# Performance work log

Measured on AMD Instinct MI355X. Metric: run time of the kernel, lower is better.

The kernel has to match this reference:

```python
import jax, jax.numpy as jnp
import numpy as np

B, N, K = 8, 4096, 64          # graphs, nodes per graph, clusters
E_PER = 65536                   # edges per graph (avg degree 16)
EPS = 1e-15


def gcn_conv(x, W, b, src, dst, num_nodes):
    """PyG GCNConv: add self-loops, symmetric deg^-1/2 normalization, sum-aggregate at dst."""
    h = x @ W
    loop = jnp.arange(num_nodes, dtype=src.dtype)
    s_all = jnp.concatenate([src, loop])
    d_all = jnp.concatenate([dst, loop])
    deg = jax.ops.segment_sum(jnp.ones(d_all.shape[0], dtype=h.dtype), d_all, num_segments=num_nodes)
    dis = jnp.where(deg > 0, jax.lax.rsqrt(deg), 0.0)
    msg = h[s_all] * (dis[s_all] * dis[d_all])[:, None]
    return jax.ops.segment_sum(msg, d_all, num_segments=num_nodes) + b


def setup_inputs() -> dict:
    key = jax.random.key(0)
    ks = jax.random.split(key, 12)
    F_in, H, F_out = 128, 128, 128
    x = jax.random.normal(ks[0], (B * N, F_in), dtype=jnp.float32)
    # within-graph random edges, then offset to global node ids
    local = jax.random.randint(ks[1], (2, B * E_PER), 0, N, dtype=jnp.int32)
    offs = jnp.repeat(jnp.arange(B, dtype=jnp.int32) * N, E_PER)
    edge_index = local + offs[None, :]
    batch = jnp.repeat(jnp.arange(B, dtype=jnp.int32), N)

    def lin(k, i, o):
        return (jax.random.normal(k, (i, o), dtype=jnp.float32) / np.float32(np.sqrt(i)))

    return {
        "x": x, "edge_index": edge_index, "batch": batch,
        "W1": lin(ks[2], F_in, H), "b1": jnp.zeros((H,), jnp.float32),
        "W2": lin(ks[3], H, H),    "b2": jnp.zeros((H,), jnp.float32),
        "Wa1": lin(ks[4], H, H),   "ba1": jnp.zeros((H,), jnp.float32),
        "Wa2": lin(ks[5], H, K),   "ba2": jnp.zeros((K,), jnp.float32),
        "Wo": lin(ks[6], H, F_out), "bo": jnp.zeros((F_out,), jnp.float32),
    }


def reference(x, edge_index, batch, W1, b1, W2, b2, Wa1, ba1, Wa2, ba2, Wo, bo):
    num_nodes = B * N
    src, dst = edge_index[0], edge_index[1]
    # two GCN layers (dropout inactive in eval mode)
    h = jax.nn.relu(gcn_conv(x, W1, b1, src, dst, num_nodes))
    h = gcn_conv(h, W2, b2, src, dst, num_nodes)
    # assignment MLP + softmax (module applies softmax; dense_mincut_pool re-applies it)
    s = jax.nn.softmax(jnp.tanh(h @ Wa1 + ba1) @ Wa2 + ba2, axis=-1)
    # to_dense_adj: scatter edges into [B, N, N]
    g = src // N
    adj = jnp.zeros((B, N, N), h.dtype).at[g, src % N, dst % N].add(1.0)
    # to_dense_batch: equal-size graphs -> reshape (mask all True)
    x_d = h.reshape(B, N, -1)
    s_d = jax.nn.softmax(s.reshape(B, N, K), axis=-1)  # PyG internal softmax (double softmax, faithful)
    # dense_mincut_pool
    out = jnp.einsum('bnk,bnf->bkf', s_d, x_d)              # s^T x : [B,K,F]
    As = jnp.einsum('bnm,bmk->bnk', adj, s_d)
    out_adj = jnp.einsum('bnk,bnj->bkj', s_d, As)           # s^T A s : [B,K,K]
    mincut_num = jnp.trace(out_adj, axis1=-2, axis2=-1)
    d_flat = adj.sum(-1)                                    # node degrees
    mincut_den = jnp.einsum('bnk,bn,bnk->b', s_d, d_flat, s_d)  # trace(s^T D s)
    mincut_loss = jnp.mean(-(mincut_num / mincut_den))
    ss = jnp.einsum('bnk,bnj->bkj', s_d, s_d)
    ss_n = jnp.linalg.norm(ss, axis=(-1, -2), keepdims=True)
    i_s = jnp.eye(K, dtype=ss.dtype)
    ortho_loss = jnp.mean(jnp.linalg.norm(ss / ss_n - i_s / jnp.sqrt(jnp.float32(K)), axis=(-1, -2)))
    # zero diagonal + symmetric degree normalization of pooled adj
    out_adj = out_adj * (1.0 - i_s)
    d = jnp.sqrt(out_adj.sum(-1))[:, None, :] + EPS         # [B,1,K]
    out_adj = out_adj / d / jnp.swapaxes(d, 1, 2)
    # output projection
    pooled_x = jax.nn.relu(out.reshape(-1, out.shape[-1]) @ Wo + bo)  # [B*K, F_out]
    pooled_batch = jnp.repeat(jnp.arange(B), K)
    # pooled_adj returned densely: pooled_edge_index == nonzero(pooled_adj > 0) (dynamic shape)
    return pooled_x, out_adj, pooled_batch, mincut_loss, ortho_loss
```

## Files before the change

kernel.cpp:

```cpp
#include <hip/hip_runtime.h>

#define NNODES 32768
#define NEDGES 524288
#define KCL 64
#define CPG 16

typedef _Float16 half8v __attribute__((ext_vector_type(8)));
typedef _Float16 half4v __attribute__((ext_vector_type(4)));
typedef float floatx4 __attribute__((ext_vector_type(4)));

#define WT1_OFF   0
#define WT2_OFF   16384
#define WTA1_OFF  32768
#define WTA2_OFF  49152
#define WTO_OFF   57344
#define WT_TOTAL  73728

__device__ __forceinline__ float wave_sum(float v) {
#pragma unroll
  for (int off = 32; off > 0; off >>= 1) v += __shfl_xor(v, off, 64);
  return v;
}

__global__ __launch_bounds__(256) void hist2_kernel(const int* __restrict__ src, const int* __restrict__ dst,
                                                    int* __restrict__ pIn,
                                                    const float* __restrict__ W1, const float* __restrict__ W2,
                                                    const float* __restrict__ Wa1, const float* __restrict__ Wa2,
                                                    const float* __restrict__ Wo, _Float16* __restrict__ wt16) {
  __shared__ int hIn[4096];
  const int t = threadIdx.x;
  const int g = blockIdx.x & 7;
  const int chunk = blockIdx.x >> 3;
  const int ebase = (g << 16) + (chunk << 12);
  const int nbase = g << 12;
  for (int i = t; i < 4096; i += 256) hIn[i] = 0;
  __syncthreads();
  {
    int tg = blockIdx.x * 256 + t;
#pragma unroll
    for (int i = 0; i < 3; i++) {
      int id = tg + i * 32768;
      if (id < WT_TOTAL) {
        const float* W; int base, BN;
        if (id < 16384)      { W = W1;  base = WT1_OFF;  BN = 128; }
        else if (id < 32768) { W = W2;  base = WT2_OFF;  BN = 128; }
        else if (id < 49152) { W = Wa1; base = WTA1_OFF; BN = 128; }
        else if (id < 57344) { W = Wa2; base = WTA2_OFF; BN = 64; }
        else                 { W = Wo;  base = WTO_OFF;  BN = 128; }
        int m = id - base;
        int k = m / BN, n = m % BN;
        wt16[base + n * 128 + k] = (_Float16)W[m];
      }
    }
  }
  const int4* dst4 = reinterpret_cast<const int4*>(dst + ebase);
#pragma unroll
  for (int i = 0; i < 4; ++i) {
    int4 d = dst4[i * 256 + t];
    atomicAdd(&hIn[d.x - nbase], 1);
    atomicAdd(&hIn[d.y - nbase], 1);
    atomicAdd(&hIn[d.z - nbase], 1);
    atomicAdd(&hIn[d.w - nbase], 1);
  }
  __syncthreads();
  int* dIn = pIn + ((size_t)(g * CPG + chunk) << 12);
  for (int i = t; i < 4096; i += 256) dIn[i] = hIn[i];
}

__global__ __launch_bounds__(1024) void scan2_kernel(const int* __restrict__ pIn, int* __restrict__ offs,
                                                     int* __restrict__ cbase, float* __restrict__ dis) {
  __shared__ int part[1024];
  const int t = threadIdx.x;
  const int g = blockIdx.x;
  int tot[4];
  int s = 0;
#pragma unroll
  for (int j = 0; j < 4; ++j) {
    int l = t * 4 + j;
    int cnt = 0;
#pragma unroll
    for (int c = 0; c < CPG; ++c) cnt += pIn[(((size_t)(g * CPG + c)) << 12) + l];
    tot[j] = cnt;
    s += cnt;
  }
  part[t] = s;
  __syncthreads();
  for (int off = 1; off < 1024; off <<= 1) {
    int add = (t >= off) ? part[t - off] : 0;
    __syncthreads();
    part[t] += add;
    __syncthreads();
  }
  int run = (g << 16) + ((t == 0) ? 0 : part[t - 1]);
#pragma unroll
  for (int j = 0; j < 4; ++j) {
    int l = t * 4 + j;
    int n = (g << 12) + l;
    offs[n] = run;
    dis[n] = rsqrtf((float)tot[j] + 1.0f);
    int running = run;
#pragma unroll
    for (int c = 0; c < CPG; ++c) {
      size_t idx = (((size_t)(g * CPG + c)) << 12) + l;
      cbase[idx] = running;
      running += pIn[idx];
    }
    run += tot[j];
  }
  if (g == 0 && t == 0) offs[NNODES] = NEDGES;
}

__global__ __launch_bounds__(256) void scatter2_kernel(const int* __restrict__ src, const int* __restrict__ dst,
                                                       const int* __restrict__ cbase, int* __restrict__ ssrc) {
  __shared__ int cur[4096];
  const int t = threadIdx.x;
  const int g = blockIdx.x & 7;
  const int chunk = blockIdx.x >> 3;
  const int ebase = (g << 16) + (chunk << 12);
  const int nbase = g << 12;
  const int* cb = cbase + ((size_t)(g * CPG + chunk) << 12);
  for (int i = t; i < 4096; i += 256) cur[i] = cb[i];
  __syncthreads();
  const int4* dst4 = reinterpret_cast<const int4*>(dst + ebase);
  const int4* src4 = reinterpret_cast<const int4*>(src + ebase);
#pragma unroll
  for (int i = 0; i < 4; ++i) {
    int4 d = dst4[i * 256 + t];
    int4 s = src4[i * 256 + t];
    int p0 = atomicAdd(&cur[d.x - nbase], 1); ssrc[p0] = s.x;
    int p1 = atomicAdd(&cur[d.y - nbase], 1); ssrc[p1] = s.y;
    int p2 = atomicAdd(&cur[d.z - nbase], 1); ssrc[p2] = s.z;
    int p3 = atomicAdd(&cur[d.w - nbase], 1); ssrc[p3] = s.w;
  }
}

template <int ACT, int BIAS, int SCALE, int AFP32>
__global__ __launch_bounds__(256) void mgemm_kernel(const void* __restrict__ Ain, const _Float16* __restrict__ WT16,
                                                    const float* __restrict__ bias, const float* __restrict__ rowscale,
                                                    _Float16* __restrict__ Cout) {
  __shared__ _Float16 WT[128][136];
  const int t = threadIdx.x;
  const int lane = t & 63;
  const int quad = lane >> 4, l16 = lane & 15;
  const long rowbase = (long)(blockIdx.x & 7) * 4096 + (long)(blockIdx.x >> 3) * 128 + (t >> 6) * 32;
  half8v af[2][4];
#pragma unroll
  for (int rt = 0; rt < 2; rt++)
#pragma unroll
    for (int kt = 0; kt < 4; kt++) {
      if (AFP32) {
        const float* A32 = (const float*)Ain;
        const float* p = A32 + (rowbase + rt * 16 + l16) * 128 + kt * 32 + quad * 8;
        float4 p0 = *reinterpret_cast<const float4*>(p);
        float4 p1 = *reinterpret_cast<const float4*>(p + 4);
        half8v h = {(_Float16)p0.x, (_Float16)p0.y, (_Float16)p0.z, (_Float16)p0.w,
                    (_Float16)p1.x, (_Float16)p1.y, (_Float16)p1.z, (_Float16)p1.w};
        af[rt][kt] = h;
      } else {
        const _Float16* A16 = (const _Float16*)Ain;
        af[rt][kt] = *reinterpret_cast<const half8v*>(A16 + (rowbase + rt * 16 + l16) * 128 + kt * 32 + quad * 8);
      }
    }
#pragma unroll
  for (int i = 0; i < 8; i++) {
    int idx = i * 256 + t;
    int n = idx >> 4, k8 = (idx & 15) << 3;
    *reinterpret_cast<half8v*>(&WT[n][k8]) = *reinterpret_cast<const half8v*>(&WT16[n * 128 + k8]);
  }
  __syncthreads();
  floatx4 acc[2][8];
#pragma unroll
  for (int rt = 0; rt < 2; rt++)
#pragma unroll
    for (int ct = 0; ct < 8; ct++) acc[rt][ct] = {0.f, 0.f, 0.f, 0.f};
#pragma unroll
  for (int kt = 0; kt < 4; kt++) {
    half8v bf[8];
#pragma unroll
    for (int ct = 0; ct < 8; ct++)
      bf[ct] = *reinterpret_cast<const half8v*>(&WT[ct * 16 + l16][kt * 32 + quad * 8]);
#pragma unroll
    for (int rt = 0; rt < 2; rt++)
#pragma unroll
      for (int ct = 0; ct < 8; ct++)
        acc[rt][ct] = __builtin_amdgcn_mfma_f32_16x16x32_f16(af[rt][kt], bf[ct], acc[rt][ct], 0, 0, 0);
  }
#pragma unroll
  for (int rt = 0; rt < 2; rt++) {
#pragma unroll
    for (int r = 0; r < 4; r++) {
      long row = rowbase + rt * 16 + quad * 4 + r;
      float sc = SCALE ? rowscale[row] : 1.f;
#pragma unroll
      for (int ct = 0; ct < 8; ct++) {
        float v = acc[rt][ct][r];
        if (SCALE) v *= sc;
        if (BIAS) v += bias[ct * 16 + l16];
        if (ACT == 1) v = fmaxf(v, 0.f);
        Cout[row * 128 + ct * 16 + l16] = (_Float16)v;
      }
    }
  }
}

__global__ __launch_bounds__(256) void mlp_kernel(const _Float16* __restrict__ h2, const _Float16* __restrict__ wta1,
                                                  const _Float16* __restrict__ wta2, const float* __restrict__ ba1,
                                                  const float* __restrict__ ba2, _Float16* __restrict__ sh) {
  __shared__ _Float16 WT1[128][136];
  __shared__ _Float16 Z[128][136];
  const int t = threadIdx.x;
  const int lane = t & 63;
  const int quad = lane >> 4, l16 = lane & 15;
  const int w = t >> 6;
  const long rowbase = (long)(blockIdx.x & 7) * 4096 + (long)(blockIdx.x >> 3) * 128 + w * 32;
  half8v af[2][4];
#pragma unroll
  for (int rt = 0; rt < 2; rt++)
#pragma unroll
    for (int kt = 0; kt < 4; kt++)
      af[rt][kt] = *reinterpret_cast<const half8v*>(h2 + (rowbase + rt * 16 + l16) * 128 + kt * 32 + quad * 8);
#pragma unroll
  for (int i = 0; i < 8; i++) {
    int idx = i * 256 + t;
    int n = idx >> 4, k8 = (idx & 15) << 3;
    *reinterpret_cast<half8v*>(&WT1[n][k8]) = *reinterpret_cast<const half8v*>(&wta1[n * 128 + k8]);
  }
  __syncthreads();
  {
    floatx4 acc[2][8];
#pragma unroll
    for (int rt = 0; rt < 2; rt++)
#pragma unroll
      for (int ct = 0; ct < 8; ct++) acc[rt][ct] = {0.f, 0.f, 0.f, 0.f};
#pragma unroll
    for (int kt = 0; kt < 4; kt++) {
      half8v bf[8];
#pragma unroll
      for (int ct = 0; ct < 8; ct++)
        bf[ct] = *reinterpret_cast<const half8v*>(&WT1[ct * 16 + l16][kt * 32 + quad * 8]);
#pragma unroll
      for (int rt = 0; rt < 2; rt++)
#pragma unroll
        for (int ct = 0; ct < 8; ct++)
          acc[rt][ct] = __builtin_amdgcn_mfma_f32_16x16x32_f16(af[rt][kt], bf[ct], acc[rt][ct], 0, 0, 0);
    }
#pragma unroll
    for (int rt = 0; rt < 2; rt++)
#pragma unroll
      for (int r = 0; r < 4; r++) {
        int lrow = w * 32 + rt * 16 + quad * 4 + r;
#pragma unroll
        for (int ct = 0; ct < 8; ct++) {
          float v = tanhf(acc[rt][ct][r] + ba1[ct * 16 + l16]);
          Z[lrow][ct * 16 + l16] = (_Float16)v;
        }
      }
  }
  __syncthreads();
#pragma unroll
  for (int i = 0; i < 4; i++) {
    int idx = i * 256 + t;
    int n = idx >> 4, k8 = (idx & 15) << 3;
    *reinterpret_cast<half8v*>(&WT1[n][k8]) = *reinterpret_cast<const half8v*>(&wta2[n * 128 + k8]);
  }
  half8v af2[2][4];
#pragma unroll
  for (int rt = 0; rt < 2; rt++)
#pragma unroll
    for (int kt = 0; kt < 4; kt++)
      af2[rt][kt] = *reinterpret_cast<const half8v*>(&Z[w * 32 + rt * 16 + l16][kt * 32 + quad * 8]);
  __syncthreads();
  floatx4 acc2[2][4];
#pragma unroll
  for (int rt = 0; rt < 2; rt++)
#pragma unroll
    for (int ct = 0; ct < 4; ct++) acc2[rt][ct] = {0.f, 0.f, 0.f, 0.f};
#pragma unroll
  for (int kt = 0; kt < 4; kt++) {
    half8v bf[4];
#pragma unroll
    for (int ct = 0; ct < 4; ct++)
      bf[ct] = *reinterpret_cast<const half8v*>(&WT1[ct * 16 + l16][kt * 32 + quad * 8]);
#pragma unroll
    for (int rt = 0; rt < 2; rt++)
#pragma unroll
      for (int ct = 0; ct < 4; ct++)
        acc2[rt][ct] = __builtin_amdgcn_mfma_f32_16x16x32_f16(af2[rt][kt], bf[ct], acc2[rt][ct], 0, 0, 0);
  }
#pragma unroll
  for (int rt = 0; rt < 2; rt++) {
#pragma unroll
    for (int r = 0; r < 4; r++) {
      long row = rowbase + rt * 16 + quad * 4 + r;
      float v[4];
#pragma unroll
      for (int ct = 0; ct < 4; ct++) v[ct] = acc2[rt][ct][r] + ba2[ct * 16 + l16];
      float m = fmaxf(fmaxf(v[0], v[1]), fmaxf(v[2], v[3]));
#pragma unroll
      for (int off = 1; off <= 8; off <<= 1) m = fmaxf(m, __shfl_xor(m, off, 64));
      float se = 0.f;
#pragma unroll
      for (int ct = 0; ct < 4; ct++) { v[ct] = __expf(v[ct] - m); se += v[ct]; }
#pragma unroll
      for (int off = 1; off <= 8; off <<= 1) se += __shfl_xor(se, off, 64);
      float inv = 1.0f / se;
#pragma unroll
      for (int ct = 0; ct < 4; ct++) v[ct] *= inv;
      float m2 = fmaxf(fmaxf(v[0], v[1]), fmaxf(v[2], v[3]));
#pragma unroll
      for (int off = 1; off <= 8; off <<= 1) m2 = fmaxf(m2, __shfl_xor(m2, off, 64));
      float se2 = 0.f;
#pragma unroll
      for (int ct = 0; ct < 4; ct++) { v[ct] = __expf(v[ct] - m2); se2 += v[ct]; }
#pragma unroll
      for (int off = 1; off <= 8; off <<= 1) se2 += __shfl_xor(se2, off, 64);
      float inv2 = 1.0f / se2;
#pragma unroll
      for (int ct = 0; ct < 4; ct++) sh[row * 64 + ct * 16 + l16] = (_Float16)(v[ct] * inv2);
    }
  }
}

__global__ __launch_bounds__(256) void aggregate_kernel(const _Float16* __restrict__ hs, const float* __restrict__ dis,
                                                        const int* __restrict__ offs, const int* __restrict__ ssrc,
                                                        const float* __restrict__ bias, _Float16* __restrict__ outh,
                                                        int relu) {
  const int lane = threadIdx.x & 63;
  const int b = blockIdx.x;
  const int node = ((b & 7) << 12) + ((b >> 3) << 2) + (threadIdx.x >> 6);
  const int q = lane >> 4;
  const int fl = (lane & 15) * 8;
  const int e0 = offs[node], e1 = offs[node + 1];
  float fa[8];
#pragma unroll
  for (int j = 0; j < 8; j++) fa[j] = 0.f;
  int e = e0;
  for (; e + 16 <= e1; e += 16) {
    int s0 = ssrc[e + q];
    int s1 = ssrc[e + 4 + q];
    int s2 = ssrc[e + 8 + q];
    int s3 = ssrc[e + 12 + q];
    half8v v0 = *reinterpret_cast<const half8v*>(hs + (size_t)s0 * 128 + fl);
    half8v v1 = *reinterpret_cast<const half8v*>(hs + (size_t)s1 * 128 + fl);
    half8v v2 = *reinterpret_cast<const half8v*>(hs + (size_t)s2 * 128 + fl);
    half8v v3 = *reinterpret_cast<const half8v*>(hs + (size_t)s3 * 128 + fl);
#pragma unroll
    for (int j = 0; j < 8; j++) fa[j] += (float)v0[j] + (float)v1[j] + (float)v2[j] + (float)v3[j];
  }
  if (e < e1) {
    int last = e1 - 1;
    int s[4]; bool m[4];
#pragma unroll
    for (int jj = 0; jj < 4; jj++) {
      int idx = e + jj * 4 + q;
      m[jj] = idx < e1;
      int sv = ssrc[idx < last ? idx : last];
      s[jj] = m[jj] ? sv : node;
    }
#pragma unroll
    for (int jj = 0; jj < 4; jj++) {
      half8v v = *reinterpret_cast<const half8v*>(hs + (size_t)s[jj] * 128 + fl);
      if (m[jj]) {
#pragma unroll
        for (int j = 0; j < 8; j++) fa[j] += (float)v[j];
      }
    }
  }
#pragma unroll
  for (int j = 0; j < 8; j++) {
    fa[j] += __shfl_xor(fa[j], 16, 64);
    fa[j] += __shfl_xor(fa[j], 32, 64);
  }
  if (q == 0) {
    float dn = dis[node];
    half8v self = *reinterpret_cast<const half8v*>(hs + (size_t)node * 128 + fl);
    float4 b0 = *reinterpret_cast<const float4*>(bias + fl);
    float4 b1 = *reinterpret_cast<const float4*>(bias + fl + 4);
    float bb[8] = {b0.x, b0.y, b0.z, b0.w, b1.x, b1.y, b1.z, b1.w};
    half8v r;
#pragma unroll
    for (int j = 0; j < 8; j++) {
      float v = fmaf(fa[j] + (float)self[j], dn, bb[j]);
      if (relu) v = fmaxf(v, 0.f);
      r[j] = (_Float16)v;
    }
    *reinterpret_cast<half8v*>(outh + (size_t)node * 128 + fl) = r;
  }
}

__global__ __launch_bounds__(256) void gather_kernel(const _Float16* __restrict__ sh, const int* __restrict__ offs,
                                                     const int* __restrict__ ssrc, _Float16* __restrict__ Gh,
                                                     float* __restrict__ dnp) {
  const int lane = threadIdx.x & 63;
  const int b = blockIdx.x;
  const int node = ((b & 7) << 12) + ((b >> 3) << 2) + (threadIdx.x >> 6);
  const int q = lane >> 3;
  const int fl = (lane & 7) * 8;
  const int e0 = offs[node], e1 = offs[node + 1];
  float fa[8];
  float sq = 0.f;
#pragma unroll
  for (int j = 0; j < 8; j++) fa[j] = 0.f;
  int e = e0;
  for (; e + 16 <= e1; e += 16) {
    int s0 = ssrc[e + q];
    int s1 = ssrc[e + 8 + q];
    half8v v0 = *reinterpret_cast<const half8v*>(sh + (size_t)s0 * 64 + fl);
    half8v v1 = *reinterpret_cast<const half8v*>(sh + (size_t)s1 * 64 + fl);
#pragma unroll
    for (int j = 0; j < 8; j++) {
      float f0 = (float)v0[j], f1 = (float)v1[j];
      fa[j] += f0 + f1;
      sq = fmaf(f0, f0, sq);
      sq = fmaf(f1, f1, sq);
    }
  }
  if (e < e1) {
    int last = e1 - 1;
    int i0 = e + q, i1 = e + 8 + q;
    bool m0 = i0 < e1, m1 = i1 < e1;
    int sv0 = ssrc[i0 < last ? i0 : last];
    int sv1 = ssrc[i1 < last ? i1 : last];
    int s0 = m0 ? sv0 : node;
    int s1 = m1 ? sv1 : node;
    half8v v0 = *reinterpret_cast<const half8v*>(sh + (size_t)s0 * 64 + fl);
    half8v v1 = *reinterpret_cast<const half8v*>(sh + (size_t)s1 * 64 + fl);
#pragma unroll
    for (int j = 0; j < 8; j++) {
      float f0 = m0 ? (float)v0[j] : 0.f;
      float f1 = m1 ? (float)v1[j] : 0.f;
      fa[j] += f0 + f1;
      sq = fmaf(f0, f0, sq);
      sq = fmaf(f1, f1, sq);
    }
  }
#pragma unroll
  for (int j = 0; j < 8; j++) {
    fa[j] += __shfl_xor(fa[j], 8, 64);
    fa[j] += __shfl_xor(fa[j], 16, 64);
    fa[j] += __shfl_xor(fa[j], 32, 64);
  }
  float den = wave_sum(sq);
  if (lane == 0) dnp[node] = den;
  if (q == 0) {
    half8v r;
#pragma unroll
    for (int j = 0; j < 8; j++) r[j] = (_Float16)fa[j];
    *reinterpret_cast<half8v*>(Gh + (size_t)node * 64 + fl) = r;
  }
}

__global__ __launch_bounds__(512) void atb_kernel(const _Float16* __restrict__ sh, const _Float16* __restrict__ Gh,
                                                  const _Float16* __restrict__ h2, float* __restrict__ pF) {
  __shared__ float Xs[32][64];
  __shared__ float Ys[32][256];
  const int t = threadIdx.x;
  const int g = blockIdx.x & 7, chunk = blockIdx.x >> 3;
  const int n0 = g * 4096 + chunk * 128;
  const int rg = t >> 6;
  const int cl = t & 63;
  float acc[8][4];
#pragma unroll
  for (int r = 0; r < 8; r++)
#pragma unroll
    for (int j = 0; j < 4; j++) acc[r][j] = 0.f;

  for (int kt = 0; kt < 4; ++kt) {
    const int nb = n0 + kt * 32;
    {
      int k = t >> 4, c = (t & 15) * 4;
      half4v hv = *reinterpret_cast<const half4v*>(&sh[(size_t)(nb + k) * 64 + c]);
      float4 val = {(float)hv[0], (float)hv[1], (float)hv[2], (float)hv[3]};
      *reinterpret_cast<float4*>(&Xs[k][c]) = val;
    }
#pragma unroll
    for (int it = 0; it < 4; ++it) {
      int slot = it * 512 + t;
      int k = slot >> 6, c = (slot & 63) * 4;
      half4v hv;
      if (c < 64)       hv = *reinterpret_cast<const half4v*>(&Gh[(size_t)(nb + k) * 64 + c]);
      else if (c < 128) hv = *reinterpret_cast<const half4v*>(&sh[(size_t)(nb + k) * 64 + (c - 64)]);
      else              hv = *reinterpret_cast<const half4v*>(&h2[(size_t)(nb + k) * 128 + (c - 128)]);
      float4 val = {(float)hv[0], (float)hv[1], (float)hv[2], (float)hv[3]};
      *reinterpret_cast<float4*>(&Ys[k][c]) = val;
    }
    __syncthreads();
#pragma unroll
    for (int k = 0; k < 32; ++k) {
      float4 b4 = *reinterpret_cast<const float4*>(&Ys[k][cl * 4]);
      float4 a0 = *reinterpret_cast<const float4*>(&Xs[k][rg * 8]);
      float4 a1 = *reinterpret_cast<const float4*>(&Xs[k][rg * 8 + 4]);
      float a[8] = {a0.x, a0.y, a0.z, a0.w, a1.x, a1.y, a1.z, a1.w};
#pragma unroll
      for (int r = 0; r < 8; r++) {
        acc[r][0] = fmaf(a[r], b4.x, acc[r][0]);
        acc[r][1] = fmaf(a[r], b4.y, acc[r][1]);
        acc[r][2] = fmaf(a[r], b4.z, acc[r][2]);
        acc[r][3] = fmaf(a[r], b4.w, acc[r][3]);
      }
    }
    __syncthreads();
  }
  float* dst = pF + (size_t)blockIdx.x * 16384;
#pragma unroll
  for (int r = 0; r < 8; r++) {
    float4 o4 = {acc[r][0], acc[r][1], acc[r][2], acc[r][3]};
    *reinterpret_cast<float4*>(&dst[(rg * 8 + r) * 256 + cl * 4]) = o4;
  }
}

__global__ __launch_bounds__(256) void merge_kernel(const float* __restrict__ pF, float* __restrict__ oadj,
                                                    float* __restrict__ ssb, _Float16* __restrict__ outp16) {
  int g = blockIdx.x & 7;
  int o4 = (blockIdx.x >> 3) * 256 + threadIdx.x;
  float sx = 0.f, sy = 0.f, sz = 0.f, sw = 0.f;
#pragma unroll
  for (int q = 0; q < 32; ++q) {
    float4 v = *reinterpret_cast<const float4*>(pF + (size_t)(q * 8 + g) * 16384 + o4 * 4);
    sx += v.x; sy += v.y; sz += v.z; sw += v.w;
  }
  int row = o4 >> 6;
  int c = (o4 & 63) * 4;
  if (c < 64) {
    float4 o = {sx, sy, sz, sw};
    *reinterpret_cast<float4*>(&oadj[g * 4096 + row * 64 + c]) = o;
  } else if (c < 128) {
    float4 o = {sx, sy, sz, sw};
    *reinterpret_cast<float4*>(&ssb[g * 4096 + row * 64 + (c - 64)]) = o;
  } else {
    half4v h = {(_Float16)sx, (_Float16)sy, (_Float16)sz, (_Float16)sw};
    *reinterpret_cast<half4v*>(&outp16[g * 8192 + row * 128 + (c - 128)]) = h;
  }
}

__global__ __launch_bounds__(256) void epilogue2_kernel(const float* __restrict__ oadj, const float* __restrict__ ssb,
                                                        const _Float16* __restrict__ outp16, const _Float16* __restrict__ wto,
                                                        const float* __restrict__ bo, const float* __restrict__ dn,
                                                        float* __restrict__ out) {
  __shared__ _Float16 outpS[64][136];
  __shared__ _Float16 WoT[128][136];
  __shared__ float red[256];
  __shared__ float rowsum[64];
  __shared__ float dw[4], w1[4], w2[4], w3[4];
  const int g = blockIdx.x, t = threadIdx.x;

#pragma unroll
  for (int i = 0; i < 8; i++) {
    int idx = i * 256 + t;
    int n = idx >> 4, k8 = (idx & 15) << 3;
    *reinterpret_cast<half8v*>(&WoT[n][k8]) = *reinterpret_cast<const half8v*>(&wto[n * 128 + k8]);
  }
#pragma unroll
  for (int i = 0; i < 4; i++) {
    int idx = i * 256 + t;
    int orow = idx >> 4, c8 = (idx & 15) * 8;
    half8v v = *reinterpret_cast<const half8v*>(&outp16[g * 8192 + orow * 128 + c8]);
    *reinterpret_cast<half8v*>(&outpS[orow][c8]) = v;
  }

  const int row = t >> 2, p = t & 3;
  float Areg[16];
  float trs_p = 0.f, ssq_p = 0.f;
#pragma unroll
  for (int c4 = 0; c4 < 4; c4++) {
    float4 a = *reinterpret_cast<const float4*>(&oadj[g * 4096 + row * 64 + p * 16 + c4 * 4]);
    Areg[c4 * 4 + 0] = a.x; Areg[c4 * 4 + 1] = a.y; Areg[c4 * 4 + 2] = a.z; Areg[c4 * 4 + 3] = a.w;
    float4 s = *reinterpret_cast<const float4*>(&ssb[g * 4096 + row * 64 + p * 16 + c4 * 4]);
    float vv[4] = {s.x, s.y, s.z, s.w};
#pragma unroll
    for (int jj = 0; jj < 4; jj++) {
      ssq_p += vv[jj] * vv[jj];
      int col = p * 16 + c4 * 4 + jj;
      if (col == row) trs_p += vv[jj];
    }
  }
  float da = 0.f;
#pragma unroll
  for (int i = 0; i < 16; i++) da += dn[g * 4096 + i * 256 + t];
  float dws = wave_sum(da);
  if ((t & 63) == 0) dw[t >> 6] = dws;

  float rs = 0.f, tra = 0.f;
#pragma unroll
  for (int c = 0; c < 16; c++) {
    int j = p * 16 + c;
    if (j == row) tra += Areg[c];
    else rs += Areg[c];
  }
  red[t] = rs;
  __syncthreads();
  if (p == 0) rowsum[row] = red[t] + red[t + 1] + red[t + 2] + red[t + 3];
  float v1 = wave_sum(tra), v2 = wave_sum(trs_p), v3 = wave_sum(ssq_p);
  if ((t & 63) == 0) { int w = t >> 6; w1[w] = v1; w2[w] = v2; w3[w] = v3; }
  __syncthreads();
  if (t == 0) {
    float TRA = w1[0] + w1[1] + w1[2] + w1[3];
    float TRS = w2[0] + w2[1] + w2[2] + w2[3];
    float SSQ = w3[0] + w3[1] + w3[2] + w3[3];
    float DEN = dw[0] + dw[1] + dw[2] + dw[3];
    atomicAdd(&out[98816], -(TRA / DEN) * 0.125f);
    float ssn = sqrtf(SSQ);
    atomicAdd(&out[98817], sqrtf(2.0f - TRS / (4.0f * ssn)) * 0.125f);
  }
  float di = sqrtf(rowsum[row]) + 1e-15f;
#pragma unroll
  for (int c = 0; c < 16; c++) {
    int j = p * 16 + c;
    float v = (j == row) ? 0.f : Areg[c];
    float dj = sqrtf(rowsum[j]) + 1e-15f;
    out[65536 + g * 4096 + row * 64 + j] = v / (di * dj);
  }
  if (t < 64) out[98304 + g * 64 + t] = (float)g;

  const int lane = t & 63;
  const int quad = lane >> 4, l16 = lane & 15;
  const int w = t >> 6;
  floatx4 acc[8];
#pragma unroll
  for (int ct = 0; ct < 8; ct++) acc[ct] = {0.f, 0.f, 0.f, 0.f};
#pragma unroll
  for (int kt = 0; kt < 4; kt++) {
    half8v af = *reinterpret_cast<const half8v*>(&outpS[w * 16 + l16][kt * 32 + quad * 8]);
#pragma unroll
    for (int ct = 0; ct < 8; ct++) {
      half8v bf = *reinterpret_cast<const half8v*>(&WoT[ct * 16 + l16][kt * 32 + quad * 8]);
      acc[ct] = __builtin_amdgcn_mfma_f32_16x16x32_f16(af, bf, acc[ct], 0, 0, 0);
    }
  }
#pragma unroll
  for (int r = 0; r < 4; r++) {
    int orow = w * 16 + quad * 4 + r;
#pragma unroll
    for (int ct = 0; ct < 8; ct++) {
      int col = ct * 16 + l16;
      float v = fmaxf(acc[ct][r] + bo[col], 0.f);
      out[(g * 64 + orow) * 128 + col] = v;
    }
  }
}

extern "C" void kernel_launch(void* const* d_in, const int* in_sizes, int n_in,
                              void* d_out, int out_size, void* d_ws, size_t ws_size,
                              hipStream_t stream) {
  const float* x   = (const float*)d_in[0];
  const int*   ei  = (const int*)d_in[1];
  const float* W1  = (const float*)d_in[3];
  const float* b1  = (const float*)d_in[4];
  const float* W2  = (const float*)d_in[5];
  const float* b2  = (const float*)d_in[6];
  const float* Wa1 = (const float*)d_in[7];
  const float* ba1 = (const float*)d_in[8];
  const float* Wa2 = (const float*)d_in[9];
  const float* ba2 = (const float*)d_in[10];
  const float* Wo  = (const float*)d_in[11];
  const float* bo  = (const float*)d_in[12];
  const int* src = ei;
  const int* dst = ei + NEDGES;
  float* out = (float*)d_out;

  char* ws = (char*)d_ws;
  size_t o = 0;
  auto alloc = [&](size_t bytes) -> void* {
    void* p = ws + o;
    o += (bytes + 255) & ~(size_t)255;
    return p;
  };
  _Float16* h16A = (_Float16*)alloc((size_t)NNODES * 128 * 2);
  _Float16* h16B = (_Float16*)alloc((size_t)NNODES * 128 * 2);
  _Float16* h16C = (_Float16*)alloc((size_t)NNODES * 128 * 2);
  _Float16* sh   = (_Float16*)alloc((size_t)NNODES * 64 * 2);
  _Float16* Gh   = (_Float16*)alloc((size_t)NNODES * 64 * 2);
  float* pF    = (float*)alloc((size_t)256 * 16384 * 4);
  float* dis   = (float*)alloc((size_t)NNODES * 4);
  int* offs    = (int*)alloc((size_t)(NNODES + 1) * 4);
  int* ssrc    = (int*)alloc((size_t)NEDGES * 4);
  int* pIn     = (int*)alloc((size_t)8 * CPG * 4096 * 4);
  int* cbase   = (int*)alloc((size_t)8 * CPG * 4096 * 4);
  float* dn    = (float*)alloc((size_t)NNODES * 4);
  float* oadj  = (float*)alloc(8 * 4096 * 4);
  float* ssb   = (float*)alloc(8 * 4096 * 4);
  _Float16* outp16 = (_Float16*)alloc(8 * 8192 * 2);
  _Float16* wt16   = (_Float16*)alloc((size_t)WT_TOTAL * 2);

  hipMemsetAsync(out + 98816, 0, 2 * sizeof(float), stream);

  hist2_kernel<<<8 * CPG, 256, 0, stream>>>(src, dst, pIn, W1, W2, Wa1, Wa2, Wo, wt16);
  scan2_kernel<<<8, 1024, 0, stream>>>(pIn, offs, cbase, dis);
  scatter2_kernel<<<8 * CPG, 256, 0, stream>>>(src, dst, cbase, ssrc);

  mgemm_kernel<0, 0, 1, 1><<<NNODES / 128, 256, 0, stream>>>(x, wt16 + WT1_OFF, nullptr, dis, h16A);
  aggregate_kernel<<<NNODES / 4, 256, 0, stream>>>(h16A, dis, offs, ssrc, b1, h16B, 1);
  mgemm_kernel<0, 0, 1, 0><<<NNODES / 128, 256, 0, stream>>>(h16B, wt16 + WT2_OFF, nullptr, dis, h16A);
  aggregate_kernel<<<NNODES / 4, 256, 0, stream>>>(h16A, dis, offs, ssrc, b2, h16C, 0);

  mlp_kernel<<<NNODES / 128, 256, 0, stream>>>(h16C, wt16 + WTA1_OFF, wt16 + WTA2_OFF, ba1, ba2, sh);

  gather_kernel<<<NNODES / 4, 256, 0, stream>>>(sh, offs, ssrc, Gh, dn);
  atb_kernel<<<256, 512, 0, stream>>>(sh, Gh, h16C, pF);
  merge_kernel<<<128, 256, 0, stream>>>(pF, oadj, ssb, outp16);
  epilogue2_kernel<<<8, 256, 0, stream>>>(oadj, ssb, outp16, wt16 + WTO_OFF, bo, dn, out);
}
```

Measured before the change: 211.7 us.

## Use MFMA for pooling A^T B kernel and halve MLP rows per block

The atb kernel, which computes s^T [G | s | h2] per 128-node chunk, now stages fp16 transposed tiles in shared memory and uses 16x16x32 f16 MFMA instructions instead of fp32 scalar FMAs. This targets that kernel's scalar ALU cost. The MLP kernel now processes 64 rows per block instead of 128, doubling the grid size and cutting register and shared memory use per block for better occupancy. In exchange, the MLP weights are reloaded into shared memory twice as often, and the atb kernel does transposed scalar shared-memory stores that may cause bank conflicts.

Result: faster. 196.8 us, median of 2 (-7.0%).

```diff
diff --git a/kernel.cpp b/kernel.cpp
--- a/kernel.cpp
+++ b/kernel.cpp
@@ -207,18 +207,16 @@
                                                   const _Float16* __restrict__ wta2, const float* __restrict__ ba1,
                                                   const float* __restrict__ ba2, _Float16* __restrict__ sh) {
   __shared__ _Float16 WT1[128][136];
-  __shared__ _Float16 Z[128][136];
+  __shared__ _Float16 Z[64][136];
   const int t = threadIdx.x;
   const int lane = t & 63;
   const int quad = lane >> 4, l16 = lane & 15;
   const int w = t >> 6;
-  const long rowbase = (long)(blockIdx.x & 7) * 4096 + (long)(blockIdx.x >> 3) * 128 + w * 32;
-  half8v af[2][4];
-#pragma unroll
-  for (int rt = 0; rt < 2; rt++)
-#pragma unroll
-    for (int kt = 0; kt < 4; kt++)
-      af[rt][kt] = *reinterpret_cast<const half8v*>(h2 + (rowbase + rt * 16 + l16) * 128 + kt * 32 + quad * 8);
+  const long rowbase = (long)(blockIdx.x & 7) * 4096 + (long)(blockIdx.x >> 3) * 64 + w * 16;
+  half8v af[4];
+#pragma unroll
+  for (int kt = 0; kt < 4; kt++)
+    af[kt] = *reinterpret_cast<const half8v*>(h2 + (rowbase + l16) * 128 + kt * 32 + quad * 8);
 #pragma unroll
   for (int i = 0; i < 8; i++) {
     int idx = i * 256 + t;
@@ -227,34 +225,26 @@
   }
   __syncthreads();
   {
-    floatx4 acc[2][8];
-#pragma unroll
-    for (int rt = 0; rt < 2; rt++)
-#pragma unroll
-      for (int ct = 0; ct < 8; ct++) acc[rt][ct] = {0.f, 0.f, 0.f, 0.f};
+    floatx4 acc[8];
+#pragma unroll
+    for (int ct = 0; ct < 8; ct++) acc[ct] = {0.f, 0.f, 0.f, 0.f};
 #pragma unroll
     for (int kt = 0; kt < 4; kt++) {
-      half8v bf[8];
-#pragma unroll
-      for (int ct = 0; ct < 8; ct++)
-        bf[ct] = *reinterpret_cast<const half8v*>(&WT1[ct * 16 + l16][kt * 32 + quad * 8]);
-#pragma unroll
-      for (int rt = 0; rt < 2; rt++)
-#pragma unroll
-        for (int ct = 0; ct < 8; ct++)
-          acc[rt][ct] = __builtin_amdgcn_mfma_f32_16x16x32_f16(af[rt][kt], bf[ct], acc[rt][ct], 0, 0, 0);
-    }
-#pragma unroll
-    for (int rt = 0; rt < 2; rt++)
-#pragma unroll
-      for (int r = 0; r < 4; r++) {
-        int lrow = w * 32 + rt * 16 + quad * 4 + r;
-#pragma unroll
-        for (int ct = 0; ct < 8; ct++) {
-          float v = tanhf(acc[rt][ct][r] + ba1[ct * 16 + l16]);
-          Z[lrow][ct * 16 + l16] = (_Float16)v;
-        }
+#pragma unroll
+      for (int ct = 0; ct < 8; ct++) {
+        half8v bf = *reinterpret_cast<const half8v*>(&WT1[ct * 16 + l16][kt * 32 + quad * 8]);
+        acc[ct] = __builtin_amdgcn_mfma_f32_16x16x32_f16(af[kt], bf, acc[ct], 0, 0, 0);
       }
+    }
+#pragma unroll
+    for (int r = 0; r < 4; r++) {
+      int lrow = w * 16 + quad * 4 + r;
+#pragma unroll
+      for (int ct = 0; ct < 8; ct++) {
+        float v = tanhf(acc[ct][r] + ba1[ct * 16 + l16]);
+        Z[lrow][ct * 16 + l16] = (_Float16)v;
+      }
+    }
   }
   __syncthreads();
 #pragma unroll
@@ -263,61 +253,50 @@
     int n = idx >> 4, k8 = (idx & 15) << 3;
     *reinterpret_cast<half8v*>(&WT1[n][k8]) = *reinterpret_cast<const half8v*>(&wta2[n * 128 + k8]);
   }
-  half8v af2[2][4];
-#pragma unroll
-  for (int rt = 0; rt < 2; rt++)
-#pragma unroll
-    for (int kt = 0; kt < 4; kt++)
-      af2[rt][kt] = *reinterpret_cast<const half8v*>(&Z[w * 32 + rt * 16 + l16][kt * 32 + quad * 8]);
-  __syncthreads();
-  floatx4 acc2[2][4];
-#pragma unroll
-  for (int rt = 0; rt < 2; rt++)
-#pragma unroll
-    for (int ct = 0; ct < 4; ct++) acc2[rt][ct] = {0.f, 0.f, 0.f, 0.f};
+  half8v af2[4];
+#pragma unroll
+  for (int kt = 0; kt < 4; kt++)
+    af2[kt] = *reinterpret_cast<const half8v*>(&Z[w * 16 + l16][kt * 32 + quad * 8]);
+  __syncthreads();
+  floatx4 acc2[4];
+#pragma unroll
+  for (int ct = 0; ct < 4; ct++) acc2[ct] = {0.f, 0.f, 0.f, 0.f};
 #pragma unroll
   for (int kt = 0; kt < 4; kt++) {
-    half8v bf[4];
-#pragma unroll
-    for (int ct = 0; ct < 4; ct++)
-      bf[ct] = *reinterpret_cast<const half8v*>(&WT1[ct * 16 + l16][kt * 32 + quad * 8]);
-#pragma unroll
-    for (int rt = 0; rt < 2; rt++)
-#pragma unroll
-      for (int ct = 0; ct < 4; ct++)
-        acc2[rt][ct] = __builtin_amdgcn_mfma_f32_16x16x32_f16(af2[rt][kt], bf[ct], acc2[rt][ct], 0, 0, 0);
-  }
-#pragma unroll
-  for (int rt = 0; rt < 2; rt++) {
-#pragma unroll
-    for (int r = 0; r < 4; r++) {
-      long row = rowbase + rt * 16 + quad * 4 + r;
-      float v[4];
-#pragma unroll
-      for (int ct = 0; ct < 4; ct++) v[ct] = acc2[rt][ct][r] + ba2[ct * 16 + l16];
-      float m = fmaxf(fmaxf(v[0], v[1]), fmaxf(v[2], v[3]));
-#pragma unroll
-      for (int off = 1; off <= 8; off <<= 1) m = fmaxf(m, __shfl_xor(m, off, 64));
-      float se = 0.f;
-#pragma unroll
-      for (int ct = 0; ct < 4; ct++) { v[ct] = __expf(v[ct] - m); se += v[ct]; }
-#pragma unroll
-      for (int off = 1; off <= 8; off <<= 1) se += __shfl_xor(se, off, 64);
-      float inv = 1.0f / se;
-#pragma unroll
-      for (int ct = 0; ct < 4; ct++) v[ct] *= inv;
-      float m2 = fmaxf(fmaxf(v[0], v[1]), fmaxf(v[2], v[3]));
-#pragma unroll
-      for (int off = 1; off <= 8; off <<= 1) m2 = fmaxf(m2, __shfl_xor(m2, off, 64));
-      float se2 = 0.f;
-#pragma unroll
-      for (int ct = 0; ct < 4; ct++) { v[ct] = __expf(v[ct] - m2); se2 += v[ct]; }
-#pragma unroll
-      for (int off = 1; off <= 8; off <<= 1) se2 += __shfl_xor(se2, off, 64);
-      float inv2 = 1.0f / se2;
-#pragma unroll
-      for (int ct = 0; ct < 4; ct++) sh[row * 64 + ct * 16 + l16] = (_Float16)(v[ct] * inv2);
-    }
+#pragma unroll
+    for (int ct = 0; ct < 4; ct++) {
+      half8v bf = *reinterpret_cast<const half8v*>(&WT1[ct * 16 + l16][kt * 32 + quad * 8]);
+      acc2[ct] = __builtin_amdgcn_mfma_f32_16x16x32_f16(af2[kt], bf, acc2[ct], 0, 0, 0);
+    }
+  }
+#pragma unroll
+  for (int r = 0; r < 4; r++) {
+    long row = rowbase + quad * 4 + r;
+    float v[4];
+#pragma unroll
+    for (int ct = 0; ct < 4; ct++) v[ct] = acc2[ct][r] + ba2[ct * 16 + l16];
+    float m = fmaxf(fmaxf(v[0], v[1]), fmaxf(v[2], v[3]));
+#pragma unroll
+    for (int off = 1; off <= 8; off <<= 1) m = fmaxf(m, __shfl_xor(m, off, 64));
+    float se = 0.f;
+#pragma unroll
+    for (int ct = 0; ct < 4; ct++) { v[ct] = __expf(v[ct] - m); se += v[ct]; }
+#pragma unroll
+    for (int off = 1; off <= 8; off <<= 1) se += __shfl_xor(se, off, 64);
+    float inv = 1.0f / se;
+#pragma unroll
+    for (int ct = 0; ct < 4; ct++) v[ct] *= inv;
+    float m2 = fmaxf(fmaxf(v[0], v[1]), fmaxf(v[2], v[3]));
+#pragma unroll
+    for (int off = 1; off <= 8; off <<= 1) m2 = fmaxf(m2, __shfl_xor(m2, off, 64));
+    float se2 = 0.f;
+#pragma unroll
+    for (int ct = 0; ct < 4; ct++) { v[ct] = __expf(v[ct] - m2); se2 += v[ct]; }
+#pragma unroll
+    for (int off = 1; off <= 8; off <<= 1) se2 += __shfl_xor(se2, off, 64);
+    float inv2 = 1.0f / se2;
+#pragma unroll
+    for (int ct = 0; ct < 4; ct++) sh[row * 64 + ct * 16 + l16] = (_Float16)(v[ct] * inv2);
   }
 }
 
@@ -452,60 +431,60 @@
 
 __global__ __launch_bounds__(512) void atb_kernel(const _Float16* __restrict__ sh, const _Float16* __restrict__ Gh,
                                                   const _Float16* __restrict__ h2, float* __restrict__ pF) {
-  __shared__ float Xs[32][64];
-  __shared__ float Ys[32][256];
+  __shared__ _Float16 XsT[64][136];
+  __shared__ _Float16 YsT[256][40];
   const int t = threadIdx.x;
   const int g = blockIdx.x & 7, chunk = blockIdx.x >> 3;
   const int n0 = g * 4096 + chunk * 128;
-  const int rg = t >> 6;
-  const int cl = t & 63;
-  float acc[8][4];
-#pragma unroll
-  for (int r = 0; r < 8; r++)
-#pragma unroll
-    for (int j = 0; j < 4; j++) acc[r][j] = 0.f;
+  const int lane = t & 63;
+  const int w = t >> 6;
+  const int mtile = w & 3;
+  const int nhalf = w >> 2;
+  const int quad = lane >> 4, l16 = lane & 15;
+
+#pragma unroll
+  for (int i = 0; i < 4; i++) {
+    int slot = i * 512 + t;
+    int k = slot >> 4, c4 = (slot & 15) * 4;
+    half4v v = *reinterpret_cast<const half4v*>(&sh[(size_t)(n0 + k) * 64 + c4]);
+#pragma unroll
+    for (int j = 0; j < 4; j++) XsT[c4 + j][k] = v[j];
+  }
+
+  floatx4 acc[8];
+#pragma unroll
+  for (int nt = 0; nt < 8; nt++) acc[nt] = {0.f, 0.f, 0.f, 0.f};
 
   for (int kt = 0; kt < 4; ++kt) {
     const int nb = n0 + kt * 32;
-    {
-      int k = t >> 4, c = (t & 15) * 4;
-      half4v hv = *reinterpret_cast<const half4v*>(&sh[(size_t)(nb + k) * 64 + c]);
-      float4 val = {(float)hv[0], (float)hv[1], (float)hv[2], (float)hv[3]};
-      *reinterpret_cast<float4*>(&Xs[k][c]) = val;
-    }
-#pragma unroll
-    for (int it = 0; it < 4; ++it) {
-      int slot = it * 512 + t;
-      int k = slot >> 6, c = (slot & 63) * 4;
-      half4v hv;
-      if (c < 64)       hv = *reinterpret_cast<const half4v*>(&Gh[(size_t)(nb + k) * 64 + c]);
-      else if (c < 128) hv = *reinterpret_cast<const half4v*>(&sh[(size_t)(nb + k) * 64 + (c - 64)]);
-      else              hv = *reinterpret_cast<const half4v*>(&h2[(size_t)(nb + k) * 128 + (c - 128)]);
-      float4 val = {(float)hv[0], (float)hv[1], (float)hv[2], (float)hv[3]};
-      *reinterpret_cast<float4*>(&Ys[k][c]) = val;
-    }
     __syncthreads();
 #pragma unroll
-    for (int k = 0; k < 32; ++k) {
-      float4 b4 = *reinterpret_cast<const float4*>(&Ys[k][cl * 4]);
-      float4 a0 = *reinterpret_cast<const float4*>(&Xs[k][rg * 8]);
-      float4 a1 = *reinterpret_cast<const float4*>(&Xs[k][rg * 8 + 4]);
-      float a[8] = {a0.x, a0.y, a0.z, a0.w, a1.x, a1.y, a1.z, a1.w};
-#pragma unroll
-      for (int r = 0; r < 8; r++) {
-        acc[r][0] = fmaf(a[r], b4.x, acc[r][0]);
-        acc[r][1] = fmaf(a[r], b4.y, acc[r][1]);
-        acc[r][2] = fmaf(a[r], b4.z, acc[r][2]);
-        acc[r][3] = fmaf(a[r], b4.w, acc[r][3]);
-      }
+    for (int i = 0; i < 4; i++) {
+      int slot = i * 512 + t;
+      int cg = slot & 15, k = (slot >> 4) & 31, ch = slot >> 9;
+      int c = ch * 64 + cg * 4;
+      half4v v;
+      if (c < 64)       v = *reinterpret_cast<const half4v*>(&Gh[(size_t)(nb + k) * 64 + c]);
+      else if (c < 128) v = *reinterpret_cast<const half4v*>(&sh[(size_t)(nb + k) * 64 + (c - 64)]);
+      else              v = *reinterpret_cast<const half4v*>(&h2[(size_t)(nb + k) * 128 + (c - 128)]);
+#pragma unroll
+      for (int j = 0; j < 4; j++) YsT[c + j][k] = v[j];
     }
     __syncthreads();
+    half8v af = *reinterpret_cast<const half8v*>(&XsT[mtile * 16 + l16][kt * 32 + quad * 8]);
+#pragma unroll
+    for (int nt = 0; nt < 8; nt++) {
+      half8v bf = *reinterpret_cast<const half8v*>(&YsT[(nhalf * 8 + nt) * 16 + l16][quad * 8]);
+      acc[nt] = __builtin_amdgcn_mfma_f32_16x16x32_f16(af, bf, acc[nt], 0, 0, 0);
+    }
   }
   float* dst = pF + (size_t)blockIdx.x * 16384;
 #pragma unroll
-  for (int r = 0; r < 8; r++) {
-    float4 o4 = {acc[r][0], acc[r][1], acc[r][2], acc[r][3]};
-    *reinterpret_cast<float4*>(&dst[(rg * 8 + r) * 256 + cl * 4]) = o4;
+  for (int nt = 0; nt < 8; nt++) {
+#pragma unroll
+    for (int r = 0; r < 4; r++) {
+      dst[(mtile * 16 + quad * 4 + r) * 256 + (nhalf * 8 + nt) * 16 + l16] = acc[nt][r];
+    }
   }
 }
 
@@ -693,7 +672,7 @@
   mgemm_kernel<0, 0, 1, 0><<<NNODES / 128, 256, 0, stream>>>(h16B, wt16 + WT2_OFF, nullptr, dis, h16A);
   aggregate_kernel<<<NNODES / 4, 256, 0, stream>>>(h16A, dis, offs, ssrc, b2, h16C, 0);
 
-  mlp_kernel<<<NNODES / 128, 256, 0, stream>>>(h16C, wt16 + WTA1_OFF, wt16 + WTA2_OFF, ba1, ba2, sh);
+  mlp_kernel<<<NNODES / 64, 256, 0, stream>>>(h16C, wt16 + WTA1_OFF, wt16 + WTA2_OFF, ba1, ba2, sh);
 
   gather_kernel<<<NNODES / 4, 256, 0, stream>>>(sh, offs, ssrc, Gh, dn);
   atb_kernel<<<256, 512, 0, stream>>>(sh, Gh, h16C, pF);
```
